# Optimization experiments

Hardware: AMD Instinct MI355X
Metric: run time of the kernel (lower is better)

The kernel has to match this reference:

```python
import jax, jax.numpy as jnp
import numpy as np

K = 32                      # nsample (neighbors)
NPTS = [4096, 2048, 1024]   # npts // downsample_ratios [1,2,4]
CH = [(6, 64, 64), (134, 128, 128), (262, 256, 256)]  # (c_in_edge, c_mid, c_out) per EdgeConv
OUT_CH = 128
EPS = 1e-5


def setup_inputs():
    key = jax.random.key(0)
    ks = iter(jax.random.split(key, 64))
    d = {"pcd": jax.random.normal(next(ks), (8, 4096, 3), dtype=jnp.float32)}
    for li, (cin, cmid, cout) in enumerate(CH, start=1):
        d[f"W{li}a"] = jax.random.normal(next(ks), (cmid, cin), dtype=jnp.float32) * 0.05
        d[f"b{li}a"] = jax.random.normal(next(ks), (cmid,), dtype=jnp.float32) * 0.01
        d[f"g{li}a"] = jnp.ones((cmid,), dtype=jnp.float32)
        d[f"be{li}a"] = jnp.zeros((cmid,), dtype=jnp.float32)
        d[f"W{li}b"] = jax.random.normal(next(ks), (cout, cmid), dtype=jnp.float32) * 0.05
        d[f"b{li}b"] = jax.random.normal(next(ks), (cout,), dtype=jnp.float32) * 0.01
        d[f"g{li}b"] = jnp.ones((cout,), dtype=jnp.float32)
        d[f"be{li}b"] = jnp.zeros((cout,), dtype=jnp.float32)
    d["fcW"] = jax.random.normal(next(ks), (OUT_CH, CH[-1][2]), dtype=jnp.float32) * 0.05
    d["fcb"] = jnp.zeros((OUT_CH,), dtype=jnp.float32)
    return d


def _knn_idx(q, p, k):
    # q: [B,m,3] queries, p: [B,n,3] points -> [B,m,k] nearest-neighbor indices
    d = (jnp.sum(q * q, -1)[:, :, None] + jnp.sum(p * p, -1)[:, None, :]
         - 2.0 * jnp.einsum('bmd,bnd->bmn', q, p))
    _, idx = jax.lax.top_k(-d, k)
    return idx


def _bn(x, g, b):
    # training-mode BatchNorm2d over [B,C,m,k], biased variance (torch behavior)
    mu = jnp.mean(x, axis=(0, 2, 3), keepdims=True)
    var = jnp.mean((x - mu) ** 2, axis=(0, 2, 3), keepdims=True)
    return (x - mu) * jax.lax.rsqrt(var + EPS) * g[None, :, None, None] + b[None, :, None, None]


def _edge_conv(xyz, feat, npoints, params):
    # xyz: [B,n,3], feat: [B,C,n] or None. Range sampling = first npoints points.
    W1, b1, g1, be1, W2, b2, g2, be2 = params
    new_xyz = xyz[:, :npoints]
    # use_xyz=True: concat features (as [B,n,C]) with xyz
    f = xyz if feat is None else jnp.concatenate([jnp.transpose(feat, (0, 2, 1)), xyz], -1)
    new_f = f[:, :npoints]                       # [B,m,D]
    idx = _knn_idx(new_xyz, xyz, K)              # [B,m,K]
    knn_f = jax.vmap(lambda a, i: a[i])(f, idx)  # [B,m,K,D] gather
    tiled = jnp.broadcast_to(new_f[:, :, None, :], knn_f.shape)
    e = jnp.concatenate([knn_f - tiled, tiled], -1)  # [B,m,K,2D] edge features
    h = jnp.einsum('bmkc,oc->bomk', e, W1) + b1[None, :, None, None]
    h = jax.nn.relu(_bn(h, g1, be1))
    h = jnp.einsum('bcmk,oc->bomk', h, W2) + b2[None, :, None, None]
    h = jax.nn.relu(_bn(h, g2, be2))
    return new_xyz, jnp.max(h, axis=-1)          # max-pool over K -> [B,C,m]


def reference(pcd, W1a, b1a, g1a, be1a, W1b, b1b, g1b, be1b,
              W2a, b2a, g2a, be2a, W2b, b2b, g2b, be2b,
              W3a, b3a, g3a, be3a, W3b, b3b, g3b, be3b, fcW, fcb):
    xyz = pcd[..., :3]
    feat = None  # pcd has only xyz channels
    layer_params = [
        (W1a, b1a, g1a, be1a, W1b, b1b, g1b, be1b),
        (W2a, b2a, g2a, be2a, W2b, b2b, g2b, be2b),
        (W3a, b3a, g3a, be3a, W3b, b3b, g3b, be3b),
    ]
    for npoints, p in zip(NPTS, layer_params):
        xyz, feat = _edge_conv(xyz, feat, npoints, p)
    out_feat = jnp.einsum('bcn,oc->bon', feat, fcW) + fcb[None, :, None]
    # Range sampling: idx chain of aranges composes to arange(NPTS[-1])
    idx = jnp.broadcast_to(jnp.arange(NPTS[-1]), (pcd.shape[0], NPTS[-1]))
    return xyz, out_feat, idx, feat
```

## Files before the change

kernel.cpp:

```cpp
#include <hip/hip_runtime.h>
#include <hip/hip_bf16.h>

#define B8 8
#define KNN 32
typedef unsigned short u16;
typedef unsigned int u32;
typedef unsigned long long u64;

typedef __attribute__((ext_vector_type(8))) _Float16 half8;
typedef __attribute__((ext_vector_type(4))) float f32x4;

static __device__ __forceinline__ u16 f2h_u(float f) {
  _Float16 h = (_Float16)f; u16 u; __builtin_memcpy(&u, &h, 2); return u;
}

static __device__ __forceinline__ u64 enc_key(float d, int id) {
  u32 u = __float_as_uint(d);
  u = (d >= 0.f) ? (u | 0x80000000u) : ~u;
  return ((u64)u << 32) | (u32)id;
}
static __device__ __forceinline__ float dec_val(u64 k) {
  u32 u = (u32)(k >> 32);
  u = (u & 0x80000000u) ? (u & 0x7fffffffu) : ~u;
  return __uint_as_float(u);
}

static __device__ __forceinline__ u64 rank64(u64 mk, int lane, u64* slk, u64* outk, float& tau) {
  slk[lane] = mk;
  int r = 0;
#pragma unroll 16
  for (int j = 0; j < 64; ++j) r += (slk[j] < mk) ? 1 : 0;
  outk[r] = mk;
  u64 res = outk[lane];
  tau = dec_val(outk[31]);
  return res;
}

static __device__ __forceinline__ void bn_from_red(int o, const float* red_s, const float* red_q,
                                                   const float* g, const float* be, float invcnt,
                                                   float* scs, float* shs) {
  float s = 0.f, q = 0.f;
#pragma unroll
  for (int i = 0; i < 16; ++i) { s += red_s[i * 256 + o]; q += red_q[i * 256 + o]; }
  float mu  = s * invcnt;
  float var = fmaxf(q * invcnt - mu * mu, 0.f);
  float scv = g[o] * rsqrtf(var + 1e-5f);
  scs[o] = scv;
  shs[o] = fmaf(-mu, scv, be[o]);
}

__global__ __launch_bounds__(256) void knn_kernel(const float* __restrict__ pcd,
                                                  int N, int M, int* __restrict__ idxout) {
  __shared__ float4 pts[1024];
  __shared__ u64 bufk[4][32];
  __shared__ u64 slk[4][64];
  __shared__ u64 outk[4][64];
  const int t = threadIdx.x;
  const int lane = t & 63, w = t >> 6;
  const int b = blockIdx.y;
  const int m = blockIdx.x * 4 + w;
  const float* base = pcd + (size_t)b * 12288;
  const float qx = base[m*3], qy = base[m*3+1], qz = base[m*3+2];
  const float ax = -2.f*qx, ay = -2.f*qy, az = -2.f*qz;

  u64 heldk; float tau; int cnt = 0;

  for (int i = t; i < 1024; i += 256) {
    const float* p = base + (size_t)i * 3;
    float x = p[0], y = p[1], z = p[2];
    pts[i] = make_float4(x, y, z, x*x + y*y + z*z);
  }
  __syncthreads();

  {
    float4 p = pts[lane];
    float r0 = fmaf(ax, p.x, fmaf(ay, p.y, fmaf(az, p.z, p.w)));
    heldk = rank64(enc_key(r0, lane), lane, slk[w], outk[w], tau);
  }

  for (int n0 = 0; n0 < N; n0 += 1024) {
    if (n0) {
      __syncthreads();
      for (int i = t; i < 1024; i += 256) {
        const float* p = base + (size_t)(n0 + i) * 3;
        float x = p[0], y = p[1], z = p[2];
        pts[i] = make_float4(x, y, z, x*x + y*y + z*z);
      }
      __syncthreads();
    }
    for (int c = 0; c < 1024; c += 256) {
      float4 p0 = pts[c + lane];
      float4 p1 = pts[c + 64 + lane];
      float4 p2 = pts[c + 128 + lane];
      float4 p3 = pts[c + 192 + lane];
      float r[4];
      r[0] = fmaf(ax, p0.x, fmaf(ay, p0.y, fmaf(az, p0.z, p0.w)));
      r[1] = fmaf(ax, p1.x, fmaf(ay, p1.y, fmaf(az, p1.z, p1.w)));
      r[2] = fmaf(ax, p2.x, fmaf(ay, p2.y, fmaf(az, p2.z, p2.w)));
      r[3] = fmaf(ax, p3.x, fmaf(ay, p3.y, fmaf(az, p3.z, p3.w)));
      if (n0 == 0 && c == 0) r[0] = 3.4e38f;
      float rmn = fminf(fminf(r[0], r[1]), fminf(r[2], r[3]));
      if (!__any(rmn < tau)) continue;
#pragma unroll
      for (int j = 0; j < 4; ++j) {
        float rr = r[j];
        if (!__any(rr < tau)) continue;
        int gid = n0 + c + j * 64 + lane;
        bool pass = rr < tau;
        while (__any(pass)) {
          u64 mk_ = __ballot(pass);
          int before = __popcll(mk_ & ((1ull << lane) - 1ull));
          int total  = __popcll(mk_);
          int room = 32 - cnt;
          if (pass && before < room) {
            bufk[w][cnt + before] = enc_key(rr, gid);
            pass = false;
          }
          if (total >= room) {
            u64 mk = (lane < 32) ? heldk : bufk[w][lane - 32];
            heldk = rank64(mk, lane, slk[w], outk[w], tau);
            cnt = 0;
            pass = pass && (rr < tau);
          } else {
            cnt += total;
          }
        }
      }
    }
  }
  if (cnt > 0) {
    int bl = lane - 32;
    u64 mk = (lane < 32) ? heldk
             : ((bl < cnt) ? bufk[w][bl]
                           : ((0xFFFFFFFFull << 32) | (0xFFFFFF00u | (u32)lane)));
    heldk = rank64(mk, lane, slk[w], outk[w], tau);
  }
  if (lane < KNN) idxout[((size_t)b * M + m) * KNN + lane] = (int)(u32)(heldk & 0xFFFFFFFFu);
}

__global__ void prep_all(
    const float* __restrict__ W1a, const float* __restrict__ W1b,
    const float* __restrict__ W2a, const float* __restrict__ W2b,
    const float* __restrict__ W3a, const float* __restrict__ W3b,
    float* __restrict__ RED,
    float* __restrict__ WAT1, float* __restrict__ WBT1, u16* __restrict__ WBH1,
    float* __restrict__ WBT2, u16* __restrict__ WAH2, u16* __restrict__ WBH2,
    float* __restrict__ WBT3, u16* __restrict__ WAH3, u16* __restrict__ WBH3)
{
  int i0 = blockIdx.x * 256 + threadIdx.x;
  int NT = gridDim.x * 256;
  for (int i = i0; i < 49152; i += NT) RED[i] = 0.f;
  for (int i = i0; i < 256; i += NT) {
    int c = i >> 6, o = i & 63;
    float w1 = (c < 3) ? W1a[o*6 + c] : 0.f;
    float w2 = (c < 3) ? W1a[o*6 + 3 + c] : 0.f;
    WAT1[i] = w1; WBT1[i] = w2 - w1;
  }
  for (int i = i0; i < 4096; i += NT) WBH1[i] = f2h_u(W1b[i]);
  for (int i = i0; i < 68*128; i += NT) {
    int c = i >> 7, o = i & 127;
    float w1 = 0.f, w2 = 0.f;
    if (c < 67) { w1 = W2a[o*134 + c]; w2 = W2a[o*134 + 67 + c]; }
    WBT2[i] = w2 - w1;
  }
  for (int i = i0; i < 128*128; i += NT) {
    int o = i >> 7, k = i & 127;
    WAH2[i] = (k < 67) ? f2h_u(W2a[o*134 + k]) : (u16)0;
  }
  for (int i = i0; i < 16384; i += NT) WBH2[i] = f2h_u(W2b[i]);
  for (int i = i0; i < 132*256; i += NT) {
    int c = i >> 8, o = i & 255;
    float w1 = 0.f, w2 = 0.f;
    if (c < 131) { w1 = W3a[o*262 + c]; w2 = W3a[o*262 + 131 + c]; }
    WBT3[i] = w2 - w1;
  }
  for (int i = i0; i < 256*192; i += NT) {
    int o = i / 192, k = i - o * 192;
    WAH3[i] = (k < 131) ? f2h_u(W3a[o*262 + k]) : (u16)0;
  }
  for (int i = i0; i < 65536; i += NT) WBH3[i] = f2h_u(W3b[i]);
}

template<int C2, int CM, int MODE>
__global__ __launch_bounds__(256) void conv_a_gemm(
    const float* __restrict__ F, size_t fbstride,
    const int* __restrict__ idx,
    const float* __restrict__ Wt,
    const float* __restrict__ bias,
    const float* __restrict__ T,
    float* __restrict__ Tout,
    float* __restrict__ red_s, float* __restrict__ red_q,
    int M)
{
  constexpr int KP = (C2 + 3) & ~3;
  constexpr int KC = (KP <= 68) ? KP : 44;
  __shared__ float At[64][KC];
  __shared__ float Wts[KC][64];
  __shared__ int ji[64];
  __shared__ float sred[4][64];
  __shared__ float qred[4][64];
  const int t = threadIdx.x;
  const int rt = blockIdx.x, ot = blockIdx.y, b = blockIdx.z;
  const int R0 = rt * 64, oc0 = ot * 64;
  const float* Fb = F + (size_t)b * fbstride;

  if (t < 64) {
    int gr = R0 + t;
    ji[t] = (MODE == 0) ? gr : idx[((size_t)b * M + (gr >> 5)) * KNN + (gr & 31)];
  }

  const int cg = t & 15, rg = t >> 4;
  const int r0 = rg * 4, c0 = cg * 4;
  float acc[4][4];
  if (MODE == 0) {
#pragma unroll
    for (int j = 0; j < 4; ++j) {
      float bv = bias[oc0 + c0 + j];
#pragma unroll
      for (int i = 0; i < 4; ++i) acc[i][j] = bv;
    }
  } else {
#pragma unroll
    for (int i = 0; i < 4; ++i) {
      const float* tp = T + ((size_t)b * M + (size_t)((R0 + r0 + i) >> 5)) * CM + oc0 + c0;
      acc[i][0] = tp[0]; acc[i][1] = tp[1]; acc[i][2] = tp[2]; acc[i][3] = tp[3];
    }
  }
  __syncthreads();

  for (int k0 = 0; k0 < KP; k0 += KC) {
    if (k0) __syncthreads();
    for (int i = t; i < KC * 64; i += 256) {
      int c = i >> 6, o = i & 63;
      Wts[c][o] = Wt[(size_t)(k0 + c) * CM + oc0 + o];
    }
    if constexpr (C2 == 3) {
      for (int i = t; i < 64 * 4; i += 256) {
        int r = i >> 2, c = i & 3;
        At[r][c] = (c < 3) ? Fb[(size_t)ji[r] * 3 + c] : 0.f;
      }
    } else {
      constexpr int C4 = KC / 4;
      for (int i = t; i < 64 * C4; i += 256) {
        int r = i / C4, c4 = i - r * C4;
        *(float4*)&At[r][c4 * 4] = *(const float4*)&Fb[(size_t)ji[r] * KP + k0 + c4 * 4];
      }
    }
    __syncthreads();

#pragma unroll 4
    for (int k = 0; k < KC; ++k) {
      const float4 w4 = *(const float4*)&Wts[k][c0];
      float a0 = At[r0][k], a1 = At[r0+1][k], a2 = At[r0+2][k], a3 = At[r0+3][k];
      acc[0][0]=fmaf(a0,w4.x,acc[0][0]); acc[0][1]=fmaf(a0,w4.y,acc[0][1]);
      acc[0][2]=fmaf(a0,w4.z,acc[0][2]); acc[0][3]=fmaf(a0,w4.w,acc[0][3]);
      acc[1][0]=fmaf(a1,w4.x,acc[1][0]); acc[1][1]=fmaf(a1,w4.y,acc[1][1]);
      acc[1][2]=fmaf(a1,w4.z,acc[1][2]); acc[1][3]=fmaf(a1,w4.w,acc[1][3]);
      acc[2][0]=fmaf(a2,w4.x,acc[2][0]); acc[2][1]=fmaf(a2,w4.y,acc[2][1]);
      acc[2][2]=fmaf(a2,w4.z,acc[2][2]); acc[2][3]=fmaf(a2,w4.w,acc[2][3]);
      acc[3][0]=fmaf(a3,w4.x,acc[3][0]); acc[3][1]=fmaf(a3,w4.y,acc[3][1]);
      acc[3][2]=fmaf(a3,w4.z,acc[3][2]); acc[3][3]=fmaf(a3,w4.w,acc[3][3]);
    }
  }

  if (MODE == 0) {
    float* op = Tout + ((size_t)b * M + R0) * (size_t)CM + oc0;
#pragma unroll
    for (int i = 0; i < 4; ++i) {
      float* p = op + (size_t)(r0 + i) * CM + c0;
      p[0]=acc[i][0]; p[1]=acc[i][1]; p[2]=acc[i][2]; p[3]=acc[i][3];
    }
  } else {
    float cs[4], cq_[4];
#pragma unroll
    for (int j = 0; j < 4; ++j) {
      float s = acc[0][j] + acc[1][j] + acc[2][j] + acc[3][j];
      float q = acc[0][j]*acc[0][j] + acc[1][j]*acc[1][j] + acc[2][j]*acc[2][j] + acc[3][j]*acc[3][j];
      s += __shfl_xor(s, 16); q += __shfl_xor(q, 16);
      s += __shfl_xor(s, 32); q += __shfl_xor(q, 32);
      cs[j] = s; cq_[j] = q;
    }
    const int wv = t >> 6;
    if ((t & 48) == 0) {
#pragma unroll
      for (int j = 0; j < 4; ++j) { sred[wv][c0 + j] = cs[j]; qred[wv][c0 + j] = cq_[j]; }
    }
    __syncthreads();
    if (t < 64) {
      float s = sred[0][t] + sred[1][t] + sred[2][t] + sred[3][t];
      float q = qred[0][t] + qred[1][t] + qred[2][t] + qred[3][t];
      int shdw = (rt & 15) * 256;
      atomicAdd(&red_s[shdw + t], s);
      atomicAdd(&red_q[shdw + t], q);
    }
  }
}

__global__ __launch_bounds__(256) void l1_convb(
    const float* __restrict__ pcd,
    const int* __restrict__ idx,
    const float* __restrict__ WAT,
    const float* __restrict__ T,
    const u16* __restrict__ Wbh,
    const float* __restrict__ bb,
    const float* __restrict__ gA, const float* __restrict__ beA,
    const float* __restrict__ redA_s, const float* __restrict__ redA_q,
    float* __restrict__ redB_s, float* __restrict__ redB_q,
    float* __restrict__ hmax)
{
  __shared__ u16 Alds[64][72];
  __shared__ u16 Wlds[64][72];
  __shared__ float xyzs[64][4];
  __shared__ float was[3][64];
  __shared__ float scs[64], shs[64];
  __shared__ int ji[64];
  const int t = threadIdx.x;
  const int lane = t & 63, w = t >> 6;
  const int wr = w >> 1, wc = w & 1;
  const int cl = lane & 15, rq = lane >> 4;
  const int rt = blockIdx.x, b = blockIdx.y;
  const int R0 = rt * 64;
  const float* pb = pcd + (size_t)b * 12288;

  if (t < 64) ji[t] = idx[((size_t)b * 4096 + ((R0 + t) >> 5)) * KNN + ((R0 + t) & 31)];
  if (t < 192) was[t / 64][t & 63] = WAT[t];
  if (t >= 192) bn_from_red(t - 192, redA_s, redA_q, gA, beA, 1.f/1048576.f, scs, shs);
  for (int i = t; i < 64 * 8; i += 256) {
    int o = i >> 3, seg = i & 7;
    *(float4*)&Wlds[o][seg * 8] = *(const float4*)&Wbh[(size_t)o * 64 + seg * 8];
  }
  __syncthreads();
  if (t < 64) {
    const float* p = pb + (size_t)ji[t] * 3;
    xyzs[t][0] = p[0]; xyzs[t][1] = p[1]; xyzs[t][2] = p[2]; xyzs[t][3] = 0.f;
  }
  __syncthreads();

  for (int i = t; i < 64 * 8; i += 256) {
    int r = i >> 3, seg = i & 7;
    float px = xyzs[r][0], py = xyzs[r][1], pz = xyzs[r][2];
    const float* Tm = T + ((size_t)b * 4096 + (size_t)((R0 + r) >> 5)) * 64;
    half8 ov;
#pragma unroll
    for (int j2 = 0; j2 < 8; ++j2) {
      int c = seg * 8 + j2;
      float hh = Tm[c];
      hh = fmaf(px, was[0][c], hh);
      hh = fmaf(py, was[1][c], hh);
      hh = fmaf(pz, was[2][c], hh);
      ov[j2] = (_Float16)fmaxf(0.f, fmaf(hh, scs[c], shs[c]));
    }
    *(half8*)&Alds[r][seg * 8] = ov;
  }
  __syncthreads();

  f32x4 acc[2][2];
#pragma unroll
  for (int fr = 0; fr < 2; ++fr)
#pragma unroll
    for (int fc = 0; fc < 2; ++fc) {
      float bv = bb[wc * 32 + fc * 16 + cl];
#pragma unroll
      for (int r = 0; r < 4; ++r) acc[fr][fc][r] = bv;
    }

#pragma unroll
  for (int kk = 0; kk < 2; ++kk) {
    half8 af[2], bf[2];
#pragma unroll
    for (int fr = 0; fr < 2; ++fr)
      af[fr] = *(const half8*)&Alds[wr*32 + fr*16 + cl][kk*32 + rq*8];
#pragma unroll
    for (int fc = 0; fc < 2; ++fc)
      bf[fc] = *(const half8*)&Wlds[wc*32 + fc*16 + cl][kk*32 + rq*8];
#pragma unroll
    for (int fr = 0; fr < 2; ++fr)
#pragma unroll
      for (int fc = 0; fc < 2; ++fc)
        acc[fr][fc] = __builtin_amdgcn_mfma_f32_16x16x32_f16(af[fr], bf[fc], acc[fr][fc], 0, 0, 0);
  }

#pragma unroll
  for (int fc = 0; fc < 2; ++fc) {
    float s = 0.f, q = 0.f, mx = -3.4e38f;
#pragma unroll
    for (int fr = 0; fr < 2; ++fr)
#pragma unroll
      for (int r = 0; r < 4; ++r) {
        float v = acc[fr][fc][r];
        s += v; q += v * v; mx = fmaxf(mx, v);
      }
    s += __shfl_xor(s, 16); q += __shfl_xor(q, 16); mx = fmaxf(mx, __shfl_xor(mx, 16));
    s += __shfl_xor(s, 32); q += __shfl_xor(q, 32); mx = fmaxf(mx, __shfl_xor(mx, 32));
    if (rq == 0) {
      int col = wc * 32 + fc * 16 + cl;
      int shdw = (rt & 15) * 256;
      atomicAdd(&redB_s[shdw + col], s);
      atomicAdd(&redB_q[shdw + col], q);
      hmax[((size_t)b * 4096 + (size_t)(rt * 2 + wr)) * 64 + col] = mx;
    }
  }
}

template<int CM, int KPAD>
__global__ __launch_bounds__(256) void conv_a_mfma(
    const float* __restrict__ F, int fstride, size_t fbstride,
    const int* __restrict__ idx, int idxstride,
    const u16* __restrict__ Wh,
    const float* __restrict__ T,
    u32* __restrict__ H32,
    float* __restrict__ red_s, float* __restrict__ red_q,
    int M)
{
  constexpr int FC = CM / 32;
  __shared__ u16 Alds[64][72];
  __shared__ u16 Wlds[CM][72];
  __shared__ int ji[64];
  const int t = threadIdx.x;
  const int lane = t & 63, w = t >> 6;
  const int wr = w >> 1, wc = w & 1;
  const int cl = lane & 15, rq = lane >> 4;
  const int rt = blockIdx.x, b = blockIdx.y;
  const int R0 = rt * 64;
  const float* Fb = F + (size_t)b * fbstride;

  if (t < 64) ji[t] = idx[((size_t)b * idxstride + ((R0 + t) >> 5)) * KNN + ((R0 + t) & 31)];

  f32x4 acc[2][FC];
#pragma unroll
  for (int fr = 0; fr < 2; ++fr)
#pragma unroll
    for (int fc = 0; fc < FC; ++fc) {
      int col = wc * (CM/2) + fc * 16 + cl;
#pragma unroll
      for (int r = 0; r < 4; ++r) {
        int row = R0 + wr*32 + fr*16 + rq*4 + r;
        acc[fr][fc][r] = T[((size_t)b * M + (row >> 5)) * CM + col];
      }
    }
  __syncthreads();

  for (int k0 = 0; k0 < KPAD; k0 += 64) {
    if (k0) __syncthreads();
    for (int i = t; i < 64 * 16; i += 256) {
      int r = i >> 4, seg = i & 15;
      int k = k0 + seg * 4;
      ushort4 s = {0,0,0,0};
      if (k < fstride) {
        float4 v = *(const float4*)&Fb[(size_t)ji[r] * fstride + k];
        s.x = f2h_u(v.x); s.y = f2h_u(v.y); s.z = f2h_u(v.z); s.w = f2h_u(v.w);
      }
      *(ushort4*)&Alds[r][seg * 4] = s;
    }
    for (int i = t; i < CM * 8; i += 256) {
      int o = i >> 3, seg = i & 7;
      *(float4*)&Wlds[o][seg * 8] = *(const float4*)&Wh[(size_t)o * KPAD + k0 + seg * 8];
    }
    __syncthreads();

#pragma unroll
    for (int kk = 0; kk < 2; ++kk) {
      half8 af[2], bf[FC];
#pragma unroll
      for (int fr = 0; fr < 2; ++fr)
        af[fr] = *(const half8*)&Alds[wr*32 + fr*16 + cl][kk*32 + rq*8];
#pragma unroll
      for (int fc = 0; fc < FC; ++fc)
        bf[fc] = *(const half8*)&Wlds[wc*(CM/2) + fc*16 + cl][kk*32 + rq*8];
#pragma unroll
      for (int fr = 0; fr < 2; ++fr)
#pragma unroll
        for (int fc = 0; fc < FC; ++fc)
          acc[fr][fc] = __builtin_amdgcn_mfma_f32_16x16x32_f16(af[fr], bf[fc], acc[fr][fc], 0, 0, 0);
    }
  }

  u32* Hb4 = H32 + ((size_t)b * ((size_t)M * KNN / 4) + (size_t)(R0 >> 2)) * CM;
#pragma unroll
  for (int fr = 0; fr < 2; ++fr)
#pragma unroll
    for (int fc = 0; fc < FC; ++fc) {
      int col = wc*(CM/2) + fc*16 + cl;
      u32 v = __builtin_amdgcn_cvt_pk_fp8_f32(acc[fr][fc][0], acc[fr][fc][1], 0, false);
      v = __builtin_amdgcn_cvt_pk_fp8_f32(acc[fr][fc][2], acc[fr][fc][3], v, true);
      Hb4[(size_t)(wr*8 + fr*4 + rq) * CM + col] = v;
    }

#pragma unroll
  for (int fc = 0; fc < FC; ++fc) {
    float s = 0.f, q = 0.f;
#pragma unroll
    for (int fr = 0; fr < 2; ++fr)
#pragma unroll
      for (int r = 0; r < 4; ++r) {
        float v = acc[fr][fc][r];
        s += v; q += v * v;
      }
    s += __shfl_xor(s, 16); q += __shfl_xor(q, 16);
    s += __shfl_xor(s, 32); q += __shfl_xor(q, 32);
    if (rq == 0) {
      int col = wc*(CM/2) + fc*16 + cl;
      int shdw = (rt & 15) * 256;
      atomicAdd(&red_s[shdw + col], s);
      atomicAdd(&red_q[shdw + col], q);
    }
  }
}

template<int CM>
__global__ __launch_bounds__(512) void conv_b_fused(
    const u32* __restrict__ H32,
    const u16* __restrict__ Wh,
    const float* __restrict__ bb,
    const float* __restrict__ gA, const float* __restrict__ beA,
    const float* __restrict__ redA_s, const float* __restrict__ redA_q, float invcnt,
    float* __restrict__ redB_s, float* __restrict__ redB_q,
    float* __restrict__ hmax,
    int Mrows)
{
  constexpr int FC = CM / 32;
  __shared__ u16 Alds[128][72];
  __shared__ u16 Wlds[CM][72];
  __shared__ float scs[CM], shs[CM];
  const int t = threadIdx.x;
  const int lane = t & 63, w = t >> 6;
  const int wr = w >> 1;
  const int wc = w & 1;
  const int cl = lane & 15, rq = lane >> 4;
  const int rt = blockIdx.x, b = blockIdx.y;
  const u32* Hb4 = H32 + ((size_t)b * ((size_t)Mrows / 4) + (size_t)(rt * 32)) * CM;

  for (int i = t; i < CM; i += 512) bn_from_red(i, redA_s, redA_q, gA, beA, invcnt, scs, shs);

  f32x4 acc[2][FC];
#pragma unroll
  for (int fr = 0; fr < 2; ++fr)
#pragma unroll
    for (int fc = 0; fc < FC; ++fc) {
      float bv = bb[wc * (CM/2) + fc * 16 + cl];
#pragma unroll
      for (int r = 0; r < 4; ++r) acc[fr][fc][r] = bv;
    }
  __syncthreads();

  for (int k0 = 0; k0 < CM; k0 += 64) {
    if (k0) __syncthreads();
    for (int i = t; i < 128 * 8; i += 512) {
      int r = i >> 3, seg = i & 7;
      int rg = r >> 2, sh8 = (r & 3) * 8;
      const u32* hp = Hb4 + (size_t)rg * CM + k0 + seg * 8;
      half8 ov;
#pragma unroll
      for (int j = 0; j < 8; ++j) {
        float v = __builtin_amdgcn_cvt_f32_fp8((hp[j] >> sh8) & 0xffu, 0);
        int c = k0 + seg * 8 + j;
        v = fmaxf(0.f, fmaf(v, scs[c], shs[c]));
        ov[j] = (_Float16)v;
      }
      *(half8*)&Alds[r][seg * 8] = ov;
    }
    for (int i = t; i < CM * 8; i += 512) {
      int o = i >> 3, seg = i & 7;
      *(float4*)&Wlds[o][seg * 8] = *(const float4*)&Wh[(size_t)o * CM + k0 + seg * 8];
    }
    __syncthreads();

#pragma unroll
    for (int kk = 0; kk < 2; ++kk) {
      half8 af[2], bf[FC];
#pragma unroll
      for (int fr = 0; fr < 2; ++fr)
        af[fr] = *(const half8*)&Alds[wr*32 + fr*16 + cl][kk*32 + rq*8];
#pragma unroll
      for (int fc = 0; fc < FC; ++fc)
        bf[fc] = *(const half8*)&Wlds[wc*(CM/2) + fc*16 + cl][kk*32 + rq*8];
#pragma unroll
      for (int fr = 0; fr < 2; ++fr)
#pragma unroll
        for (int fc = 0; fc < FC; ++fc)
          acc[fr][fc] = __builtin_amdgcn_mfma_f32_16x16x32_f16(af[fr], bf[fc], acc[fr][fc], 0, 0, 0);
    }
  }

#pragma unroll
  for (int fc = 0; fc < FC; ++fc) {
    float s = 0.f, q = 0.f, mx = -3.4e38f;
#pragma unroll
    for (int fr = 0; fr < 2; ++fr)
#pragma unroll
      for (int r = 0; r < 4; ++r) {
        float v = acc[fr][fc][r];
        s += v; q += v * v; mx = fmaxf(mx, v);
      }
    s += __shfl_xor(s, 16); q += __shfl_xor(q, 16); mx = fmaxf(mx, __shfl_xor(mx, 16));
    s += __shfl_xor(s, 32); q += __shfl_xor(q, 32); mx = fmaxf(mx, __shfl_xor(mx, 32));
    if (rq == 0) {
      int col = wc*(CM/2) + fc*16 + cl;
      int shdw = (rt & 15) * 256;
      atomicAdd(&redB_s[shdw + col], s);
      atomicAdd(&redB_q[shdw + col], q);
      hmax[((size_t)b * (Mrows >> 5) + (size_t)(rt * 4 + wr)) * CM + col] = mx;
    }
  }
}

__global__ __launch_bounds__(256) void bnrelu_fb(const float* __restrict__ hm,
    const float* __restrict__ gB, const float* __restrict__ beB,
    const float* __restrict__ redB_s, const float* __restrict__ redB_q, float invcnt,
    const float* __restrict__ pcd,
    float* __restrict__ fout, int CM, int fostride, size_t fobstride, int M) {
  __shared__ float scs[256], shs[256];
  for (int o = threadIdx.x; o < CM; o += 256) bn_from_red(o, redB_s, redB_q, gB, beB, invcnt, scs, shs);
  __syncthreads();
  int i = blockIdx.x * 256 + threadIdx.x;
  int cq = CM >> 2;
  int total = B8 * M * cq;
  if (i >= total) return;
  int c4 = i % cq; int r = i / cq;
  int b = r / M, m = r - b * M;
  float4 v = *(const float4*)&hm[((size_t)b * M + m) * CM + c4 * 4];
  int c = c4 * 4;
  float4 o;
  o.x = fmaxf(0.f, fmaf(v.x, scs[c],   shs[c]));
  o.y = fmaxf(0.f, fmaf(v.y, scs[c+1], shs[c+1]));
  o.z = fmaxf(0.f, fmaf(v.z, scs[c+2], shs[c+2]));
  o.w = fmaxf(0.f, fmaf(v.w, scs[c+3], shs[c+3]));
  float* op = fout + (size_t)b * fobstride + (size_t)m * fostride;
  *(float4*)(op + c) = o;
  if (pcd && c4 == 0) {
    const float* p = pcd + ((size_t)b * 4096 + m) * 3;
    *(float4*)(op + CM) = make_float4(p[0], p[1], p[2], 0.f);
  }
}

__global__ __launch_bounds__(256) void fc_out(const float* __restrict__ f4,
                                              const float* __restrict__ fcW, const float* __restrict__ fcb,
                                              float* __restrict__ out1, float* __restrict__ out3) {
  __shared__ float tile[32 * 257];
  const int t = threadIdx.x, b = blockIdx.x, n0 = blockIdx.y * 32;
  for (int i = t; i < 32 * 256; i += 256) {
    int n = i >> 8, c = i & 255;
    tile[n * 257 + c] = f4[((size_t)b * 1024 + n0 + n) * 256 + c];
  }
  __syncthreads();
  const int n = t & 31, og = t >> 5;
#pragma unroll
  for (int ci = 0; ci < 32; ++ci) {
    int c = og * 32 + ci;
    out3[((size_t)b * 256 + c) * 1024 + n0 + n] = tile[n * 257 + c];
  }
#pragma unroll
  for (int oi = 0; oi < 16; ++oi) {
    int o = og * 16 + oi;
    float acc = fcb[o];
    const float* w = fcW + (size_t)o * 256;
#pragma unroll 4
    for (int c = 0; c < 256; ++c) acc = fmaf(tile[n * 257 + c], w[c], acc);
    out1[((size_t)b * 128 + o) * 1024 + n0 + n] = acc;
  }
}

__global__ void out_xyz_idx(const float* __restrict__ pcd, float* __restrict__ out0,
                            float* __restrict__ out2) {
  int i = blockIdx.x * 256 + threadIdx.x;
  if (i < B8 * 1024) {
    int b = i >> 10, n = i & 1023;
    const float* p = pcd + ((size_t)b * 4096 + n) * 3;
    float* o = out0 + (size_t)i * 3;
    o[0] = p[0]; o[1] = p[1]; o[2] = p[2];
    out2[i] = (float)n;
  }
}

extern "C" void kernel_launch(void* const* d_in, const int* in_sizes, int n_in,
                              void* d_out, int out_size, void* d_ws, size_t ws_size,
                              hipStream_t stream) {
  (void)in_sizes; (void)n_in; (void)out_size; (void)ws_size;
  const float* pcd = (const float*)d_in[0];
  const float* W1a = (const float*)d_in[1];  const float* b1a = (const float*)d_in[2];
  const float* g1a = (const float*)d_in[3];  const float* be1a= (const float*)d_in[4];
  const float* W1b = (const float*)d_in[5];  const float* b1b = (const float*)d_in[6];
  const float* g1b = (const float*)d_in[7];  const float* be1b= (const float*)d_in[8];
  const float* W2a = (const float*)d_in[9];  const float* b2a = (const float*)d_in[10];
  const float* g2a = (const float*)d_in[11]; const float* be2a= (const float*)d_in[12];
  const float* W2b = (const float*)d_in[13]; const float* b2b = (const float*)d_in[14];
  const float* g2b = (const float*)d_in[15]; const float* be2b= (const float*)d_in[16];
  const float* W3a = (const float*)d_in[17]; const float* b3a = (const float*)d_in[18];
  const float* g3a = (const float*)d_in[19]; const float* be3a= (const float*)d_in[20];
  const float* W3b = (const float*)d_in[21]; const float* b3b = (const float*)d_in[22];
  const float* g3b = (const float*)d_in[23]; const float* be3b= (const float*)d_in[24];
  const float* fcW = (const float*)d_in[25]; const float* fcb = (const float*)d_in[26];

  float* wsf = (float*)d_ws;
  float* FB2 = wsf;
  float* FB3 = FB2 + 2228224;
  float* FB4 = FB3 + 2162688;
  float* TBUF= FB4 + 2097152;
  float* RED = TBUF + 2097152;
  float* R1A = RED;          float* R1B = RED + 8192;
  float* R2A = RED + 16384;  float* R2B = RED + 24576;
  float* R3A = RED + 32768;  float* R3B = RED + 40960;
  float* WAT1 = RED + 49152;
  float* WBT1 = WAT1 + 256;
  float* WBT2 = WBT1 + 256;
  float* WBT3 = WBT2 + 8704;
  float* HMAX = WBT3 + 33792;
  int* IDX1 = (int*)(HMAX + 2097152);
  int* IDX3 = IDX1 + (size_t)8 * 4096 * 32;
  u32* H32  = (u32*)(IDX3 + (size_t)8 * 1024 * 32);
  u16* WBH1 = (u16*)(H32 + 16777216);
  u16* WAH2 = WBH1 + 4096;
  u16* WBH2 = WAH2 + 16384;
  u16* WAH3 = WBH2 + 16384;
  u16* WBH3 = WAH3 + 49152;

  float* out0 = (float*)d_out;
  float* out1 = out0 + 24576;
  float* out2 = out1 + 1048576;
  float* out3 = out2 + 8192;

  prep_all<<<64, 256, 0, stream>>>(W1a, W1b, W2a, W2b, W3a, W3b, RED,
                                   WAT1, WBT1, WBH1, WBT2, WAH2, WBH2, WBT3, WAH3, WBH3);

  knn_kernel<<<dim3(1024, 8), 256, 0, stream>>>(pcd, 4096, 4096, IDX1);
  conv_a_gemm<3,64,0><<<dim3(64,1,8),256,0,stream>>>(pcd,(size_t)12288,nullptr,WBT1,b1a,nullptr,TBUF,nullptr,nullptr,4096);
  conv_a_gemm<3,64,1><<<dim3(2048,1,8),256,0,stream>>>(pcd,(size_t)12288,IDX1,WAT1,nullptr,TBUF,nullptr,R1A,R1A+4096,4096);
  l1_convb<<<dim3(2048,8),256,0,stream>>>(pcd,IDX1,WAT1,TBUF,WBH1,b1b,g1a,be1a,R1A,R1A+4096,R1B,R1B+4096,HMAX);
  bnrelu_fb<<<2048,256,0,stream>>>(HMAX,g1b,be1b,R1B,R1B+4096,1.f/1048576.f,pcd,FB2,64,68,(size_t)278528,4096);

  conv_a_gemm<67,128,0><<<dim3(32,2,8),256,0,stream>>>(FB2,(size_t)278528,nullptr,WBT2,b2a,nullptr,TBUF,nullptr,nullptr,2048);
  conv_a_mfma<128,128><<<dim3(1024,8),256,0,stream>>>(FB2,68,(size_t)278528,IDX1,4096,WAH2,TBUF,H32,R2A,R2A+4096,2048);
  conv_b_fused<128><<<dim3(512,8),512,0,stream>>>(H32,WBH2,b2b,g2a,be2a,R2A,R2A+4096,1.f/524288.f,R2B,R2B+4096,HMAX,2048*32);
  bnrelu_fb<<<2048,256,0,stream>>>(HMAX,g2b,be2b,R2B,R2B+4096,1.f/524288.f,pcd,FB3,128,132,(size_t)270336,2048);

  knn_kernel<<<dim3(256, 8), 256, 0, stream>>>(pcd, 2048, 1024, IDX3);
  conv_a_gemm<131,256,0><<<dim3(16,4,8),256,0,stream>>>(FB3,(size_t)270336,nullptr,WBT3,b3a,nullptr,TBUF,nullptr,nullptr,1024);
  conv_a_mfma<256,192><<<dim3(512,8),256,0,stream>>>(FB3,132,(size_t)270336,IDX3,1024,WAH3,TBUF,H32,R3A,R3A+4096,1024);
  conv_b_fused<256><<<dim3(256,8),512,0,stream>>>(H32,WBH3,b3b,g3a,be3a,R3A,R3A+4096,1.f/262144.f,R3B,R3B+4096,HMAX,1024*32);
  bnrelu_fb<<<2048,256,0,stream>>>(HMAX,g3b,be3b,R3B,R3B+4096,1.f/262144.f,nullptr,FB4,256,256,(size_t)262144,1024);

  fc_out<<<dim3(8, 32), 256, 0, stream>>>(FB4, fcW, fcb, out1, out3);
  out_xyz_idx<<<32, 256, 0, stream>>>(pcd, out0, out2);
}
```

Measured before the change: 753.5 us.

## Store intermediate per-point features as fp16 instead of fp32

```diff
diff --git a/kernel.cpp b/kernel.cpp
--- a/kernel.cpp
+++ b/kernel.cpp
@@ -12,6 +12,9 @@
 
 static __device__ __forceinline__ u16 f2h_u(float f) {
   _Float16 h = (_Float16)f; u16 u; __builtin_memcpy(&u, &h, 2); return u;
+}
+static __device__ __forceinline__ float h2f_u(u16 u) {
+  _Float16 h; __builtin_memcpy(&h, &u, 2); return (float)h;
 }
 
 static __device__ __forceinline__ u64 enc_key(float d, int id) {
@@ -181,9 +184,9 @@
   for (int i = i0; i < 65536; i += NT) WBH3[i] = f2h_u(W3b[i]);
 }
 
-template<int C2, int CM, int MODE>
+template<int C2, int CM, int MODE, int F16>
 __global__ __launch_bounds__(256) void conv_a_gemm(
-    const float* __restrict__ F, size_t fbstride,
+    const void* __restrict__ F, int frs, size_t fbstride,
     const int* __restrict__ idx,
     const float* __restrict__ Wt,
     const float* __restrict__ bias,
@@ -202,7 +205,6 @@
   const int t = threadIdx.x;
   const int rt = blockIdx.x, ot = blockIdx.y, b = blockIdx.z;
   const int R0 = rt * 64, oc0 = ot * 64;
-  const float* Fb = F + (size_t)b * fbstride;
 
   if (t < 64) {
     int gr = R0 + t;
@@ -235,15 +237,28 @@
       Wts[c][o] = Wt[(size_t)(k0 + c) * CM + oc0 + o];
     }
     if constexpr (C2 == 3) {
+      const float* Fb = (const float*)F + (size_t)b * fbstride;
       for (int i = t; i < 64 * 4; i += 256) {
         int r = i >> 2, c = i & 3;
         At[r][c] = (c < 3) ? Fb[(size_t)ji[r] * 3 + c] : 0.f;
       }
-    } else {
+    } else if constexpr (F16) {
+      const u16* Fb = (const u16*)F + (size_t)b * fbstride;
       constexpr int C4 = KC / 4;
       for (int i = t; i < 64 * C4; i += 256) {
         int r = i / C4, c4 = i - r * C4;
-        *(float4*)&At[r][c4 * 4] = *(const float4*)&Fb[(size_t)ji[r] * KP + k0 + c4 * 4];
+        ushort4 v = *(const ushort4*)&Fb[(size_t)ji[r] * frs + k0 + c4 * 4];
+        At[r][c4*4]   = h2f_u(v.x);
+        At[r][c4*4+1] = h2f_u(v.y);
+        At[r][c4*4+2] = h2f_u(v.z);
+        At[r][c4*4+3] = h2f_u(v.w);
+      }
+    } else {
+      const float* Fb = (const float*)F + (size_t)b * fbstride;
+      constexpr int C4 = KC / 4;
+      for (int i = t; i < 64 * C4; i += 256) {
+        int r = i / C4, c4 = i - r * C4;
+        *(float4*)&At[r][c4 * 4] = *(const float4*)&Fb[(size_t)ji[r] * frs + k0 + c4 * 4];
       }
     }
     __syncthreads();
@@ -404,7 +419,7 @@
 
 template<int CM, int KPAD>
 __global__ __launch_bounds__(256) void conv_a_mfma(
-    const float* __restrict__ F, int fstride, size_t fbstride,
+    const u16* __restrict__ F, int frs, size_t fbstride,
     const int* __restrict__ idx, int idxstride,
     const u16* __restrict__ Wh,
     const float* __restrict__ T,
@@ -422,7 +437,7 @@
   const int cl = lane & 15, rq = lane >> 4;
   const int rt = blockIdx.x, b = blockIdx.y;
   const int R0 = rt * 64;
-  const float* Fb = F + (size_t)b * fbstride;
+  const u16* Fb = F + (size_t)b * fbstride;
 
   if (t < 64) ji[t] = idx[((size_t)b * idxstride + ((R0 + t) >> 5)) * KNN + ((R0 + t) & 31)];
 
@@ -446,10 +461,7 @@
       int r = i >> 4, seg = i & 15;
       int k = k0 + seg * 4;
       ushort4 s = {0,0,0,0};
-      if (k < fstride) {
-        float4 v = *(const float4*)&Fb[(size_t)ji[r] * fstride + k];
-        s.x = f2h_u(v.x); s.y = f2h_u(v.y); s.z = f2h_u(v.z); s.w = f2h_u(v.w);
-      }
+      if (k < frs) s = *(const ushort4*)&Fb[(size_t)ji[r] * frs + k];
       *(ushort4*)&Alds[r][seg * 4] = s;
     }
     for (int i = t; i < CM * 8; i += 256) {
@@ -608,7 +620,7 @@
     const float* __restrict__ gB, const float* __restrict__ beB,
     const float* __restrict__ redB_s, const float* __restrict__ redB_q, float invcnt,
     const float* __restrict__ pcd,
-    float* __restrict__ fout, int CM, int fostride, size_t fobstride, int M) {
+    u16* __restrict__ fout, int CM, int fostride, size_t fobstride, int M) {
   __shared__ float scs[256], shs[256];
   for (int o = threadIdx.x; o < CM; o += 256) bn_from_red(o, redB_s, redB_q, gB, beB, invcnt, scs, shs);
   __syncthreads();
@@ -620,27 +632,33 @@
   int b = r / M, m = r - b * M;
   float4 v = *(const float4*)&hm[((size_t)b * M + m) * CM + c4 * 4];
   int c = c4 * 4;
-  float4 o;
-  o.x = fmaxf(0.f, fmaf(v.x, scs[c],   shs[c]));
-  o.y = fmaxf(0.f, fmaf(v.y, scs[c+1], shs[c+1]));
-  o.z = fmaxf(0.f, fmaf(v.z, scs[c+2], shs[c+2]));
-  o.w = fmaxf(0.f, fmaf(v.w, scs[c+3], shs[c+3]));
-  float* op = fout + (size_t)b * fobstride + (size_t)m * fostride;
-  *(float4*)(op + c) = o;
+  ushort4 o;
+  o.x = f2h_u(fmaxf(0.f, fmaf(v.x, scs[c],   shs[c])));
+  o.y = f2h_u(fmaxf(0.f, fmaf(v.y, scs[c+1], shs[c+1])));
+  o.z = f2h_u(fmaxf(0.f, fmaf(v.z, scs[c+2], shs[c+2])));
+  o.w = f2h_u(fmaxf(0.f, fmaf(v.w, scs[c+3], shs[c+3])));
+  u16* op = fout + (size_t)b * fobstride + (size_t)m * fostride;
+  *(ushort4*)(op + c) = o;
   if (pcd && c4 == 0) {
     const float* p = pcd + ((size_t)b * 4096 + m) * 3;
-    *(float4*)(op + CM) = make_float4(p[0], p[1], p[2], 0.f);
-  }
-}
-
-__global__ __launch_bounds__(256) void fc_out(const float* __restrict__ f4,
+    half8 xz;
+    xz[0] = (_Float16)p[0]; xz[1] = (_Float16)p[1]; xz[2] = (_Float16)p[2];
+    xz[3] = (_Float16)0.f; xz[4] = (_Float16)0.f; xz[5] = (_Float16)0.f;
+    xz[6] = (_Float16)0.f; xz[7] = (_Float16)0.f;
+    *(half8*)(op + CM) = xz;
+  }
+}
+
+__global__ __launch_bounds__(256) void fc_out(const u16* __restrict__ f4,
                                               const float* __restrict__ fcW, const float* __restrict__ fcb,
                                               float* __restrict__ out1, float* __restrict__ out3) {
   __shared__ float tile[32 * 257];
   const int t = threadIdx.x, b = blockIdx.x, n0 = blockIdx.y * 32;
-  for (int i = t; i < 32 * 256; i += 256) {
-    int n = i >> 8, c = i & 255;
-    tile[n * 257 + c] = f4[((size_t)b * 1024 + n0 + n) * 256 + c];
+  for (int i = t; i < 32 * 64; i += 256) {
+    int n = i >> 6, c4 = i & 63;
+    ushort4 v = *(const ushort4*)&f4[((size_t)b * 1024 + n0 + n) * 256 + c4 * 4];
+    float* tp = &tile[n * 257 + c4 * 4];
+    tp[0] = h2f_u(v.x); tp[1] = h2f_u(v.y); tp[2] = h2f_u(v.z); tp[3] = h2f_u(v.w);
   }
   __syncthreads();
   const int n = t & 31, og = t >> 5;
@@ -691,11 +709,11 @@
   const float* g3b = (const float*)d_in[23]; const float* be3b= (const float*)d_in[24];
   const float* fcW = (const float*)d_in[25]; const float* fcb = (const float*)d_in[26];
 
-  float* wsf = (float*)d_ws;
-  float* FB2 = wsf;
-  float* FB3 = FB2 + 2228224;
-  float* FB4 = FB3 + 2162688;
-  float* TBUF= FB4 + 2097152;
+  u16* FB2h = (u16*)d_ws;
+  u16* FB3h = FB2h + 2359296;
+  u16* FB4h = FB3h + 2228224;
+  float* wsf = (float*)(FB4h + 2097152);
+  float* TBUF= wsf;
   float* RED = TBUF + 2097152;
   float* R1A = RED;          float* R1B = RED + 8192;
   float* R2A = RED + 16384;  float* R2B = RED + 24576;
@@ -723,22 +741,22 @@
                                    WAT1, WBT1, WBH1, WBT2, WAH2, WBH2, WBT3, WAH3, WBH3);
 
   knn_kernel<<<dim3(1024, 8), 256, 0, stream>>>(pcd, 4096, 4096, IDX1);
-  conv_a_gemm<3,64,0><<<dim3(64,1,8),256,0,stream>>>(pcd,(size_t)12288,nullptr,WBT1,b1a,nullptr,TBUF,nullptr,nullptr,4096);
-  conv_a_gemm<3,64,1><<<dim3(2048,1,8),256,0,stream>>>(pcd,(size_t)12288,IDX1,WAT1,nullptr,TBUF,nullptr,R1A,R1A+4096,4096);
+  conv_a_gemm<3,64,0,0><<<dim3(64,1,8),256,0,stream>>>(pcd,3,(size_t)12288,nullptr,WBT1,b1a,nullptr,TBUF,nullptr,nullptr,4096);
+  conv_a_gemm<3,64,1,0><<<dim3(2048,1,8),256,0,stream>>>(pcd,3,(size_t)12288,IDX1,WAT1,nullptr,TBUF,nullptr,R1A,R1A+4096,4096);
   l1_convb<<<dim3(2048,8),256,0,stream>>>(pcd,IDX1,WAT1,TBUF,WBH1,b1b,g1a,be1a,R1A,R1A+4096,R1B,R1B+4096,HMAX);
-  bnrelu_fb<<<2048,256,0,stream>>>(HMAX,g1b,be1b,R1B,R1B+4096,1.f/1048576.f,pcd,FB2,64,68,(size_t)278528,4096);
-
-  conv_a_gemm<67,128,0><<<dim3(32,2,8),256,0,stream>>>(FB2,(size_t)278528,nullptr,WBT2,b2a,nullptr,TBUF,nullptr,nullptr,2048);
-  conv_a_mfma<128,128><<<dim3(1024,8),256,0,stream>>>(FB2,68,(size_t)278528,IDX1,4096,WAH2,TBUF,H32,R2A,R2A+4096,2048);
+  bnrelu_fb<<<2048,256,0,stream>>>(HMAX,g1b,be1b,R1B,R1B+4096,1.f/1048576.f,pcd,FB2h,64,72,(size_t)294912,4096);
+
+  conv_a_gemm<67,128,0,1><<<dim3(32,2,8),256,0,stream>>>(FB2h,72,(size_t)294912,nullptr,WBT2,b2a,nullptr,TBUF,nullptr,nullptr,2048);
+  conv_a_mfma<128,128><<<dim3(1024,8),256,0,stream>>>(FB2h,72,(size_t)294912,IDX1,4096,WAH2,TBUF,H32,R2A,R2A+4096,2048);
   conv_b_fused<128><<<dim3(512,8),512,0,stream>>>(H32,WBH2,b2b,g2a,be2a,R2A,R2A+4096,1.f/524288.f,R2B,R2B+4096,HMAX,2048*32);
-  bnrelu_fb<<<2048,256,0,stream>>>(HMAX,g2b,be2b,R2B,R2B+4096,1.f/524288.f,pcd,FB3,128,132,(size_t)270336,2048);
+  bnrelu_fb<<<2048,256,0,stream>>>(HMAX,g2b,be2b,R2B,R2B+4096,1.f/524288.f,pcd,FB3h,128,136,(size_t)278528,2048);
 
   knn_kernel<<<dim3(256, 8), 256, 0, stream>>>(pcd, 2048, 1024, IDX3);
-  conv_a_gemm<131,256,0><<<dim3(16,4,8),256,0,stream>>>(FB3,(size_t)270336,nullptr,WBT3,b3a,nullptr,TBUF,nullptr,nullptr,1024);
-  conv_a_mfma<256,192><<<dim3(512,8),256,0,stream>>>(FB3,132,(size_t)270336,IDX3,1024,WAH3,TBUF,H32,R3A,R3A+4096,1024);
+  conv_a_gemm<131,256,0,1><<<dim3(16,4,8),256,0,stream>>>(FB3h,136,(size_t)278528,nullptr,WBT3,b3a,nullptr,TBUF,nullptr,nullptr,1024);
+  conv_a_mfma<256,192><<<dim3(512,8),256,0,stream>>>(FB3h,136,(size_t)278528,IDX3,1024,WAH3,TBUF,H32,R3A,R3A+4096,1024);
   conv_b_fused<256><<<dim3(256,8),512,0,stream>>>(H32,WBH3,b3b,g3a,be3a,R3A,R3A+4096,1.f/262144.f,R3B,R3B+4096,HMAX,1024*32);
-  bnrelu_fb<<<2048,256,0,stream>>>(HMAX,g3b,be3b,R3B,R3B+4096,1.f/262144.f,nullptr,FB4,256,256,(size_t)262144,1024);
-
-  fc_out<<<dim3(8, 32), 256, 0, stream>>>(FB4, fcW, fcb, out1, out3);
+  bnrelu_fb<<<2048,256,0,stream>>>(HMAX,g3b,be3b,R3B,R3B+4096,1.f/262144.f,nullptr,FB4h,256,256,(size_t)262144,1024);
+
+  fc_out<<<dim3(8, 32), 256, 0, stream>>>(FB4h, fcW, fcb, out1, out3);
   out_xyz_idx<<<32, 256, 0, stream>>>(pcd, out0, out2);
 }
```

Result: no change. 749.2 us (-0.6%).
